# Kernel tuning notes

Hardware: AMD Instinct MI355X
Metric: run time of the kernel (lower is better)

Reference implementation:

```python
import jax, jax.numpy as jnp
from jax import lax
import numpy as np

H = W = 224
N = H * W
T = 25          # landscape sample points
K_MAX = 2       # number of landscapes
M_PTS = 64      # max persistence-diagram points kept (top persistence)
OUT_F = 50
CHUNK = 512     # pixels per DTM chunk


def _make_offsets(m0):
    # static, sorted-by-distance local window covering >= m0 fraction of mass for near-uniform weights
    r = int(np.ceil(np.sqrt(m0 * N / np.pi) * 1.3))
    dy, dx = np.meshgrid(np.arange(-r, r + 1), np.arange(-r, r + 1), indexing="ij")
    d2 = (dy * dy + dx * dx).astype(np.float32).ravel()
    o = np.argsort(d2, kind="stable")
    return jnp.asarray(dy.ravel()[o]), jnp.asarray(dx.ravel()[o]), jnp.asarray(d2[o]), r

_OFF = {m0: _make_offsets(m0) for m0 in (0.05, 0.2)}


def _dtm(w_img, m0):
    """Weighted distance-to-measure on the unit-spacing 224x224 grid.
    dtm(x)^2 = (1/(m0*W)) * sum of w_j * d_j^2 over nearest grid points until cumulative
    weight reaches m0*W (partial weight on the crossing point). Offsets are pre-sorted by
    distance (identical for every pixel), so no per-pixel sort is needed."""
    dy, dx, d2, r = _OFF[m0]
    B = w_img.shape[0]
    wp = jnp.pad(w_img, ((0, 0), (r, r), (r, r)))
    thr = m0 * w_img.sum(axis=(1, 2))                      # (B,)
    pix = jnp.arange(N).reshape(N // CHUNK, CHUNK)

    def body(p):
        y = p // W + r
        x = p % W + r
        vals = wp[:, y[:, None] + dy[None, :], x[:, None] + dx[None, :]]  # (B,C,O)
        c = jnp.cumsum(vals, axis=-1)
        used = jnp.minimum(jnp.maximum(thr[:, None, None] - (c - vals), 0.0), vals)
        return jnp.einsum("bco,o->bc", used, d2) / thr[:, None]

    dtm2 = lax.map(jax.checkpoint(body), pix)              # (n_chunks, B, CHUNK)
    return jnp.sqrt(jnp.maximum(dtm2.transpose(1, 0, 2).reshape(B, N), 0.0))


def _h0_pairs_np(f_batch):
    """0-dim persistent homology (sublevel filtration, 4-connectivity) via union-find.
    Returns indices of birth/death pixels so birth/death VALUES can be gathered
    differentiably in jax (PLLay-style gradients)."""
    f_batch = np.asarray(f_batch)
    B = f_batch.shape[0]
    b_idx = np.zeros((B, M_PTS), np.int32)
    d_idx = np.zeros((B, M_PTS), np.int32)
    mask = np.zeros((B, M_PTS), np.bool_)
    for bb in range(B):
        f = f_batch[bb]
        order = np.argsort(f, kind="stable")
        parent = np.full(N, -1, np.int64)
        pairs = []
        for i in order:
            i = int(i)
            parent[i] = i
            y, x = divmod(i, W)
            nbs = []
            if y > 0: nbs.append(i - W)
            if y < H - 1: nbs.append(i + W)
            if x > 0: nbs.append(i - 1)
            if x < W - 1: nbs.append(i + 1)
            for nb in nbs:
                if parent[nb] < 0:
                    continue
                ri = i
                while parent[ri] != ri:
                    parent[ri] = parent[parent[ri]]; ri = parent[ri]
                rn = nb
                while parent[rn] != rn:
                    parent[rn] = parent[parent[rn]]; rn = parent[rn]
                if ri == rn:
                    continue
                if f[ri] <= f[rn]:
                    elder, young = ri, rn
                else:
                    elder, young = rn, ri
                pairs.append((young, i))   # elder rule: younger component dies here
                parent[young] = elder
        pairs.append((int(np.argmin(f)), int(np.argmax(f))))  # essential class
        pa = np.asarray(pairs, np.int64)
        pers = f[pa[:, 1]] - f[pa[:, 0]]
        keep = np.argsort(-pers)[:M_PTS]
        k = len(keep)
        b_idx[bb, :k] = pa[keep, 0]
        d_idx[bb, :k] = pa[keep, 1]
        mask[bb, :k] = pers[keep] > 0
    return b_idx, d_idx, mask


def _topo_layer(x_img, m0, tseq, gw, gb):
    # AdTopoLayer: DTM -> H0 persistence diagram -> persistence landscapes at tseq -> Linear
    dt = _dtm(x_img, m0)                                   # (B, N)
    B = dt.shape[0]
    shapes = (jax.ShapeDtypeStruct((B, M_PTS), np.int32),
              jax.ShapeDtypeStruct((B, M_PTS), np.int32),
              jax.ShapeDtypeStruct((B, M_PTS), np.bool_))
    b_idx, d_idx, mask = jax.pure_callback(_h0_pairs_np, shapes, lax.stop_gradient(dt))
    birth = jnp.take_along_axis(dt, b_idx, axis=1)         # differentiable gather
    death = jnp.take_along_axis(dt, d_idx, axis=1)
    death = jnp.where(mask, death, birth)                  # invalid slots -> zero tent
    t = tseq[None, None, :]                                # (1,1,T)
    tents = jnp.maximum(jnp.minimum(t - birth[:, :, None], death[:, :, None] - t), 0.0)
    lam, _ = lax.top_k(tents.transpose(0, 2, 1), K_MAX)    # (B,T,K): k-th largest tents
    feat = lam.transpose(0, 2, 1).reshape(B, K_MAX * T)    # (B,50)
    return feat @ gw.T + gb


def _forward(input, params):
    xs = []
    for m0, g in ((0.05, "1"), (0.2, "2")):
        for c in range(3):
            n = "t" + g + str(c + 1)
            xs.append(_topo_layer(input[:, c], m0, params[n + "_tseq"], params[n + "_w"], params[n + "_b"]))
    x = jnp.concatenate(xs, axis=-1)                       # (B, 300)
    signal = jnp.abs(lax.stop_gradient(x)).sum(axis=0)     # (300,) detached signal
    output = jax.nn.relu(x) @ params["fc_w"].T + params["fc_b"]
    return output, signal


def setup_inputs():
    key = jax.random.key(0)
    ks = jax.random.split(key, 8)
    B = 2
    inp = {"input": jax.random.uniform(ks[0], (B, 3, H, W), jnp.float32)}
    centers = {"1": 20.0, "2": 40.0}   # typical DTM value ranges for m0=0.05 / 0.2
    i = 1
    for g in ("1", "2"):
        for c in ("1", "2", "3"):
            n = "t" + g + c
            kk = jax.random.fold_in(ks[1], i)
            inp[n + "_tseq"] = jnp.linspace(centers[g] - 15.0, centers[g] + 15.0, T).astype(jnp.float32)
            inp[n + "_w"] = 0.1 * jax.random.normal(kk, (OUT_F, K_MAX * T), jnp.float32)
            inp[n + "_b"] = jnp.zeros((OUT_F,), jnp.float32)
            i += 1
    inp["fc_w"] = 0.1 * jax.random.normal(ks[2], (7, 6 * OUT_F), jnp.float32)
    inp["fc_b"] = jnp.zeros((7,), jnp.float32)
    return inp


def reference(input, t11_tseq, t11_w, t11_b, t12_tseq, t12_w, t12_b, t13_tseq, t13_w, t13_b, t21_tseq, t21_w, t21_b, t22_tseq, t22_w, t22_b, t23_tseq, t23_w, t23_b, fc_w, fc_b):
    params = dict(t11_tseq=t11_tseq, t11_w=t11_w, t11_b=t11_b,
                  t12_tseq=t12_tseq, t12_w=t12_w, t12_b=t12_b,
                  t13_tseq=t13_tseq, t13_w=t13_w, t13_b=t13_b,
                  t21_tseq=t21_tseq, t21_w=t21_w, t21_b=t21_b,
                  t22_tseq=t22_tseq, t22_w=t22_w, t22_b=t22_b,
                  t23_tseq=t23_tseq, t23_w=t23_w, t23_b=t23_b,
                  fc_w=fc_w, fc_b=fc_b)
    return _forward(input, params)
```

## Files before the change

### kernel.cpp

```cpp
#include <hip/hip_runtime.h>
#include <stdint.h>

#define HWDIM 224
#define NPIX (HWDIM*HWDIM)
#define NFIELD 12
#define TT 25

#define R1v 37
#define PW1v (HWDIM + 2*R1v)
#define R2v 74
#define PW2v (HWDIM + 2*R2v)

#define HSIZE 16384
#define FCAP 4096
#define RHASH 4096
#define DON 36

typedef unsigned long long u64;

struct LayerParams {
    const float* tseq[6];
    const float* gw[6];
    const float* gb[6];
};

constexpr size_t alup(size_t x) { return (x + 255) & ~(size_t)255; }
constexpr size_t SZPA = (size_t)6*PW1v*(PW1v+1)*4;
constexpr size_t SZPB = (size_t)6*PW2v*(PW2v+1)*4;
constexpr size_t OFF_SUMS = 0;
constexpr size_t OFF_P0A = alup(OFF_SUMS + 8*4);
constexpr size_t OFF_PZA = alup(OFF_P0A + SZPA);
constexpr size_t OFF_P0B = alup(OFF_PZA + 2*SZPA);
constexpr size_t OFF_PZB = alup(OFF_P0B + SZPB);
constexpr size_t OFF_DT   = alup(OFF_PZB + 2*SZPB);
constexpr size_t OFF_KEY  = alup(OFF_DT   + (size_t)NFIELD*NPIX*4);
constexpr size_t OFF_HP   = alup(OFF_KEY  + (size_t)NFIELD*NPIX*8);
constexpr size_t OFF_HB   = alup(OFF_HP   + (size_t)NFIELD*HSIZE*8);
constexpr size_t OFF_X    = alup(OFF_HB   + (size_t)NFIELD*HSIZE*8);


__global__ __launch_bounds__(1024) void k_sums(const float* __restrict__ inp, float* __restrict__ sums) {
    int img = blockIdx.x;
    const float* p = inp + (size_t)img * NPIX;
    __shared__ float red[1024];
    float s = 0.f;
    for (int i = threadIdx.x; i < NPIX; i += 1024) s += p[i];
    red[threadIdx.x] = s; __syncthreads();
    for (int w = 512; w > 0; w >>= 1) {
        if (threadIdx.x < w) red[threadIdx.x] += red[threadIdx.x + w];
        __syncthreads();
    }
    if (threadIdx.x == 0) sums[img] = red[0];
}

__global__ __launch_bounds__(64) void k_prefix(const float* __restrict__ inp,
        float* __restrict__ p0a, float2* __restrict__ pza,
        float* __restrict__ p0b, float2* __restrict__ pzb) {
    int bidx = blockIdx.x;
    const int tot0 = 6 * PW1v;
    int g = (bidx >= tot0);
    int rem = g ? (bidx - tot0) : bidx;
    const int PW = g ? PW2v : PW1v, R = g ? R2v : R1v, C = PW + 1;
    int img = rem / PW, row = rem % PW;
    float* P0 = (g ? p0b : p0a) + ((size_t)img*PW + row) * C;
    float2* PZ = (g ? pzb : pza) + ((size_t)img*PW + row) * C;
    int iy = row - R;
    bool rowok = ((unsigned)iy < HWDIM);
    const float* src = inp + (size_t)img*NPIX + (size_t)(rowok ? iy : 0)*HWDIM;
    const int lane = threadIdx.x;
    if (lane == 0) { P0[0] = 0.f; PZ[0] = make_float2(0.f, 0.f); }
    float c0 = 0.f, c1 = 0.f, c2 = 0.f;
    for (int i = 0; i < 6; ++i) {
        int k = i*64 + lane;
        float v = 0.f;
        if (k < PW && rowok) { int ix = k - R; if ((unsigned)ix < HWDIM) v = src[ix]; }
        float xd = (float)k;
        float w0 = v, w1 = v*xd, w2 = v*xd*xd;
        #pragma unroll
        for (int off = 1; off < 64; off <<= 1) {
            float t0 = __shfl_up(w0, off), t1 = __shfl_up(w1, off), t2 = __shfl_up(w2, off);
            if (lane >= off) { w0 += t0; w1 += t1; w2 += t2; }
        }
        if (k < PW) {
            P0[k+1] = c0 + w0;
            PZ[k+1] = make_float2(c1 + w1, c2 + w2);
        }
        c0 += __shfl(w0, 63); c1 += __shfl(w1, 63); c2 += __shfl(w2, 63);
    }
}

__device__ __forceinline__ int k_init_exact(int X, int R) {
    int K = (int)sqrtf((float)X) + 1;
    if (K > R) K = R;
    while (K > 0 && K*K > X) --K;
    return K;
}

__device__ __forceinline__ float dmass1(int X, const float* __restrict__ P0, int bidx,
        int C, int R) {
    float m = 0.f;
    int K = 0;
    if (X >= 0) {
        K = k_init_exact(X, R);
        m = P0[bidx+K+1] - P0[bidx-K];
    }
    int t = X - 1, step = 3;
    const float* __restrict__ Pu = P0 - C;
    const float* __restrict__ Pd = P0 + C;
    for (int dyy = 1; dyy <= R; ++dyy) {
        if (__all(t < 0)) break;
        if (t >= 0) {
            while (K*K > t) --K;
            int A = bidx + K + 1, B = bidx - K;
            m += (Pu[A] - Pu[B]) + (Pd[A] - Pd[B]);
        }
        t -= step; step += 2; Pu -= C; Pd += C;
    }
    return m;
}

__global__ __launch_bounds__(256) void k_dtm(const float* __restrict__ sums,
        const float* __restrict__ p0a, const float2* __restrict__ pza,
        const float* __restrict__ p0b, const float2* __restrict__ pzb,
        float* __restrict__ dt, u64* __restrict__ key) {
    const int xcd = blockIdx.x & 7, slot = blockIdx.x >> 3;
    int f, blk;
    if (xcd < 6) {
        if (slot < 196)            { f = 6 + xcd; blk = slot; }
        else if (slot < 196 + DON) { f = xcd; blk = (196 - DON) + (slot - 196); }
        else return;
    } else {
        const int per = 196 - DON;
        if (slot >= 3*per) return;
        int q = slot / per;
        f = (xcd - 6)*3 + q; blk = slot - q*per;
    }
    const int layer = f >> 1, b = f & 1;
    const int g = layer / 3, c = layer % 3;
    const int img = b*3 + c;
    const int R = g ? R2v : R1v, PW = g ? PW2v : PW1v, C = PW + 1;
    const int R2 = 2*R*R;
    const float thr = (g ? 0.2f : 0.05f) * sums[img];
    const float* __restrict__ P0 = (g ? p0b : p0a) + (size_t)img*PW*C;
    const float2* __restrict__ PZ = (g ? pzb : pza) + (size_t)img*PW*C;

    const int p = blk*256 + threadIdx.x;
    const int y = p / HWDIM, x = p % HWDIM;
    const int xc = x + R;
    const int bidx = (y + R)*C + xc;

    const int NP = g ? 7 : 6;
    const int WSTOP = g ? 86 : 43;
    int lo = 0, hi = R2 + 1;
    for (int it = 0; it < NP; ++it) {
        int X = (lo + hi) >> 1;
        float m = dmass1(X, P0, bidx, C, R);
        if (m >= thr) hi = X; else lo = X + 1;
    }
    for (int rit = 0; rit < 14; ++rit) {
        bool act = (hi == R2 + 1) ? (lo < hi) : (hi - lo > WSTOP);
        if (__all(!act)) break;
        int X = act ? ((lo + hi) >> 1) : -1;
        float m = dmass1(X, P0, bidx, C, R);
        if (X >= 0) { if (m >= thr) hi = X; else lo = X + 1; }
    }
    const bool nr = (hi == R2 + 1);
    const int  Dst = nr ? lo : ((lo + hi) >> 1);
    const bool cross = nr ? (lo <= R2) : true;
    const int  Xin = cross ? (Dst - 1) : R2;

    float m_in = 0.f, ws = 0.f;
    const float c2n = -2.f * (float)xc;
    const int xc2i = xc * xc;
    int K = 0;
    if (Xin >= 0) {
        K = k_init_exact(Xin, R);
        int A = bidx+K+1, B = bidx-K;
        float s0 = P0[A] - P0[B]; float2 zA = PZ[A], zB = PZ[B];
        m_in += s0; ws += fmaf((float)xc2i, s0, fmaf(c2n, zA.x - zB.x, zA.y - zB.y));
    }
    {
        int t = Xin - 1, step = 3, d2 = 1;
        const float* __restrict__ Pu = P0 - C;
        const float* __restrict__ Pd = P0 + C;
        const float2* __restrict__ Zu = PZ - C;
        const float2* __restrict__ Zd = PZ + C;
        for (int dyy = 1; dyy <= R; ++dyy) {
            if (__all(t < 0)) break;
            if (t >= 0) {
                while (K*K > t) --K;
                int A = bidx+K+1, B = bidx-K;
                float c1 = (float)(d2 + xc2i);
                { float s0 = Pu[A]-Pu[B]; float2 zA = Zu[A], zB = Zu[B];
                  m_in += s0; ws += fmaf(c1, s0, fmaf(c2n, zA.x - zB.x, zA.y - zB.y)); }
                { float s0 = Pd[A]-Pd[B]; float2 zA = Zd[A], zB = Zd[B];
                  m_in += s0; ws += fmaf(c1, s0, fmaf(c2n, zA.x - zB.x, zA.y - zB.y)); }
            }
            t -= step; d2 += step; step += 2;
            Pu -= C; Pd += C; Zu -= C; Zd += C;
        }
    }
    float s = cross ? (ws + (float)Dst * (thr - m_in)) : ws;
    float d = sqrtf(fmaxf(s / thr, 0.f));
    dt[(size_t)f*NPIX + p] = d;
    key[(size_t)f*NPIX + p] = ((u64)__float_as_uint(d) << 32) | (unsigned)p;
}

__device__ inline unsigned hash64(u64 x) {
    x ^= x >> 33; x *= 0xff51afd7ed558ccdULL;
    x ^= x >> 33; x *= 0xc4ceb9fe1a85ec53ULL;
    x ^= x >> 33;
    return (unsigned)x;
}

struct FinSh {
    u64 ek[FCAP];
    unsigned int epk[FCAP];
    unsigned int eab[FCAP];
    unsigned short eru[FCAP];
    int rhk[RHASH];
    short ufp[RHASH];
    float rdt[RHASH];
    unsigned int pyd[FCAP];
    float ppr[FCAP];
};

__device__ __forceinline__ void bitonic_n(u64* ek, int tid, int n, int bst) {
    for (int k = 2; k <= n; k <<= 1) {
        for (int j = k >> 1; j > 0; j >>= 1) {
            for (int i = tid; i < n; i += bst) {
                int ixj = i ^ j;
                if (ixj > i) {
                    u64 a = ek[i], b = ek[ixj];
                    if (((i & k) == 0) ? (a > b) : (a < b)) { ek[i] = b; ek[ixj] = a; }
                }
            }
            __syncthreads();
        }
    }
}

__global__ __launch_bounds__(1024) void k_fused(const float* __restrict__ dt,
        const u64* __restrict__ key,
        u64* __restrict__ hpair, u64* __restrict__ hbest,
        LayerParams lp, float* __restrict__ xbuf) {
    const int xcd = blockIdx.x & 7, slot = blockIdx.x >> 3;
    int f;
    if (xcd < 6) { if (slot != 0) return; f = 6 + xcd; }
    else f = (xcd - 6)*3 + slot;
    const int layer = f >> 1, bb = f & 1;
    const int tid = threadIdx.x; const int bs = 1024;
    const float* dtf = dt + (size_t)f*NPIX;
    const u64* kf = key + (size_t)f*NPIX;
    u64* hp = hpair + (size_t)f*HSIZE;
    u64* hb = hbest + (size_t)f*HSIZE;

    __shared__ union U {
        unsigned short par[NPIX];
        FinSh fin;
    } sh;
    __shared__ float birth[64], death[64], featsh[2*TT];
    __shared__ int spec_a[64], spec_b[64];
    __shared__ u64 spec_e[64];
    __shared__ int cnt_s, pc_s;
    __shared__ int gmin_s, gmax_s; __shared__ float gminf_s, gmaxf_s;

    u64 mymin = ~0ull, mymax = 0;
    for (int p = tid; p < NPIX; p += bs) {
        u64 kp = kf[p]; u64 best = kp; int bi = p;
        const int y = p / HWDIM, x = p % HWDIM;
        if (y > 0)        { u64 t = kf[p - HWDIM]; if (t < best) { best = t; bi = p - HWDIM; } }
        if (y < HWDIM-1)  { u64 t = kf[p + HWDIM]; if (t < best) { best = t; bi = p + HWDIM; } }
        if (x > 0)        { u64 t = kf[p - 1];     if (t < best) { best = t; bi = p - 1; } }
        if (x < HWDIM-1)  { u64 t = kf[p + 1];     if (t < best) { best = t; bi = p + 1; } }
        sh.par[p] = (unsigned short)bi;
        if (kp < mymin) mymin = kp;
        u64 mk = (kp & 0xFFFFFFFF00000000ull) | (0xFFFFu - (unsigned)(kp & 0xFFFFu));
        if (mk > mymax) mymax = mk;
    }
    {
        u64* red = (u64*)sh.fin.pyd;
        red[tid] = mymin; red[1024 + tid] = mymax;
        __syncthreads();
        for (int w = 512; w > 0; w >>= 1) {
            if (tid < w) {
                if (red[tid + w] < red[tid]) red[tid] = red[tid + w];
                if (red[1024 + tid + w] > red[1024 + tid]) red[1024 + tid] = red[1024 + tid + w];
            }
            __syncthreads();
        }
        if (tid == 0) {
            gmin_s = (int)(unsigned)(red[0] & 0xFFFFu);
            gminf_s = __uint_as_float((unsigned)(red[0] >> 32));
            gmax_s = 0xFFFF - (int)(unsigned)(red[1024] & 0xFFFFu);
            gmaxf_s = __uint_as_float((unsigned)(red[1024] >> 32));
            cnt_s = 0; pc_s = 0;
        }
    }
    __syncthreads();
    for (int pass = 0; pass < 6; ++pass) {
        for (int p = tid; p < NPIX; p += bs) sh.par[p] = sh.par[sh.par[p]];
        __syncthreads();
    }
    for (int p = tid; p < NPIX; p += bs) {
        int a = sh.par[p];
        int n = sh.par[a];
        while (n != a) { a = n; n = sh.par[a]; }
        sh.par[p] = (unsigned short)a;
    }
    __syncthreads();
    for (int p = tid; p < NPIX; p += bs) {
        const int rp = sh.par[p];
        const int y = p / HWDIM, x = p % HWDIM;
        const u64 kp = kf[p];
        #pragma unroll
        for (int e = 0; e < 2; ++e) {
            int q;
            if (e == 0) { if (x >= HWDIM-1) continue; q = p + 1; }
            else        { if (y >= HWDIM-1) continue; q = p + HWDIM; }
            int rq = sh.par[q];
            if (rq == rp) continue;
            u64 kq = kf[q];
            u64 kmax; int ru;
            if (kp > kq) { kmax = kp; ru = rp; } else { kmax = kq; ru = rq; }
            u64 ekv = (kmax & 0xFFFFFFFF00000000ull) | ((kmax & 0xFFFFull) << 16) | (unsigned)ru;
            int ra = min(rp, rq), rb = max(rp, rq);
            u64 pk = ((u64)(unsigned)ra << 32) | (unsigned)rb;
            unsigned h = hash64(pk) & (HSIZE - 1);
            for (int probe = 0; probe < HSIZE; ++probe) {
                u64 old = atomicCAS(&hp[h], ~0ull, pk);
                if (old == ~0ull || old == pk) { atomicMin(&hb[h], ekv); break; }
                h = (h + 1) & (HSIZE - 1);
            }
        }
    }
    __syncthreads();
    for (int i = tid; i < RHASH; i += bs) sh.fin.rhk[i] = -1;
    __syncthreads();
    for (int i = tid; i < HSIZE; i += bs) {
        u64 pk = hp[i];
        if (pk != ~0ull) {
            int slot2 = atomicAdd(&cnt_s, 1);
            if (slot2 < FCAP) {
                u64 e = hb[i];
                unsigned u = (unsigned)((e >> 16) & 0xFFFFu);
                unsigned ru = (unsigned)(e & 0xFFFFu);
                sh.fin.ek[slot2] = (e & 0xFFFFFFFF00000000ull) | ((u64)u << 16) | (unsigned)slot2;
                int ra = (int)(pk >> 32), rb = (int)(pk & 0xFFFFFFFFu);
                sh.fin.epk[slot2] = ((unsigned)ra << 16) | (unsigned)rb;
                sh.fin.eru[slot2] = (unsigned short)ru;
                #pragma unroll
                for (int pass = 0; pass < 2; ++pass) {
                    int r = pass ? rb : ra;
                    unsigned h = ((unsigned)r * 2654435761u) & (RHASH - 1);
                    for (int pr = 0; pr < RHASH; ++pr) {
                        int old = atomicCAS(&sh.fin.rhk[h], -1, r);
                        if (old == -1 || old == r) break;
                        h = (h + 1) & (RHASH - 1);
                    }
                }
            }
        }
    }
    __syncthreads();
    int cnt = min(cnt_s, FCAP);
    int n1 = 64; while (n1 < cnt) n1 <<= 1;
    for (int s2 = tid; s2 < cnt; s2 += bs) {
        unsigned pk2 = sh.fin.epk[s2];
        int ra = (int)(pk2 >> 16), rb = (int)(pk2 & 0xFFFFu);
        int ru = sh.fin.eru[s2];
        int rv = (ru == ra) ? rb : ra;
        int su = -1, sv = -1;
        { unsigned h = ((unsigned)ru * 2654435761u) & (RHASH - 1);
          for (int pr = 0; pr < RHASH; ++pr) { int v = sh.fin.rhk[h]; if (v == ru) { su = (int)h; break; } if (v == -1) break; h = (h + 1) & (RHASH - 1); } }
        { unsigned h = ((unsigned)rv * 2654435761u) & (RHASH - 1);
          for (int pr = 0; pr < RHASH; ++pr) { int v = sh.fin.rhk[h]; if (v == rv) { sv = (int)h; break; } if (v == -1) break; h = (h + 1) & (RHASH - 1); } }
        sh.fin.eab[s2] = ((unsigned)su << 16) | (unsigned)(sv & 0xFFFF);
    }
    for (int i = cnt + tid; i < n1; i += bs) sh.fin.ek[i] = ~0ull;
    for (int s2 = tid; s2 < RHASH; s2 += bs) {
        sh.fin.ufp[s2] = (short)s2;
        int r = sh.fin.rhk[s2];
        sh.fin.rdt[s2] = (r >= 0) ? dtf[r] : 0.f;
    }
    __syncthreads();

    bitonic_n(sh.fin.ek, tid, n1, bs);

    if (tid < 64) {
        int pc = 0;
        for (int base = 0; base < cnt; base += 64) {
            int i = base + tid;
            int sa = -1, sb = -1; u64 e = ~0ull;
            if (i < cnt) {
                e = sh.fin.ek[i];
                int idx = (int)(e & 0xFFFFu);
                unsigned ab = sh.fin.eab[idx];
                sa = (int)(ab >> 16); sb = (int)(ab & 0xFFFFu);
                if (sa != 0xFFFF && sb != 0xFFFF) {
                    while (sh.fin.ufp[sa] != sa) { short g2 = sh.fin.ufp[sh.fin.ufp[sa]]; sh.fin.ufp[sa] = g2; sa = g2; }
                    while (sh.fin.ufp[sb] != sb) { short g2 = sh.fin.ufp[sh.fin.ufp[sb]]; sh.fin.ufp[sb] = g2; sb = g2; }
                    if (sa == sb) sa = -1;
                } else { sa = -1; }
            }
            spec_a[tid] = sa; spec_b[tid] = sb; spec_e[tid] = e;
            if (tid == 0) {
                int lim = min(64, cnt - base);
                for (int j = 0; j < lim; ++j) {
                    int sa2 = spec_a[j];
                    if (sa2 < 0) continue;
                    int sb2 = spec_b[j];
                    u64 e2 = spec_e[j];
                    while (sh.fin.ufp[sa2] != sa2) { short g2 = sh.fin.ufp[sh.fin.ufp[sa2]]; sh.fin.ufp[sa2] = g2; sa2 = g2; }
                    while (sh.fin.ufp[sb2] != sb2) { short g2 = sh.fin.ufp[sh.fin.ufp[sb2]]; sh.fin.ufp[sb2] = g2; sb2 = g2; }
                    if (sa2 == sb2) continue;
                    float fa = sh.fin.rdt[sa2], fb = sh.fin.rdt[sb2];
                    int elder, young;
                    if (fa <= fb) { elder = sa2; young = sb2; } else { elder = sb2; young = sa2; }
                    sh.fin.ufp[young] = (short)elder;
                    float pers = __uint_as_float((unsigned)(e2 >> 32)) - sh.fin.rdt[young];
                    if (pers > 0.f && pc < FCAP - 1) {
                        int u = (int)((e2 >> 16) & 0xFFFFu);
                        sh.fin.pyd[pc] = ((unsigned)sh.fin.rhk[young] << 16) | (unsigned)u;
                        sh.fin.ppr[pc] = pers; ++pc;
                    }
                }
            }
        }
        if (tid == 0) {
            sh.fin.pyd[pc] = ((unsigned)gmin_s << 16) | (unsigned)gmax_s;
            sh.fin.ppr[pc] = gmaxf_s - gminf_s; ++pc;
            pc_s = pc;
        }
    }
    __syncthreads();
    const int pc = pc_s;
    int n2 = 64; while (n2 < pc) n2 <<= 1;

    for (int i = tid; i < n2; i += bs) {
        if (i < pc && sh.fin.ppr[i] > 0.f)
            sh.fin.ek[i] = ((u64)(0xFFFFFFFFu - __float_as_uint(sh.fin.ppr[i])) << 32) | (unsigned)i;
        else sh.fin.ek[i] = ~0ull;
    }
    __syncthreads();
    bitonic_n(sh.fin.ek, tid, n2, bs);
    if (tid < 64) {
        u64 e = sh.fin.ek[tid];
        int bpix = 0, dpix = 0, msk = 0;
        if (e != ~0ull) {
            int i = (int)(e & 0xFFFFFFFFu);
            unsigned pd2 = sh.fin.pyd[i];
            bpix = (int)(pd2 >> 16); dpix = (int)(pd2 & 0xFFFFu); msk = 1;
        }
        float bv = dtf[bpix];
        float dv = msk ? dtf[dpix] : bv;
        birth[tid] = bv; death[tid] = dv;
    }
    __syncthreads();
    if (tid < TT) {
        float t = lp.tseq[layer][tid];
        float m1 = 0.f, m2 = 0.f;
        for (int m = 0; m < 64; ++m) {
            float v = fmaxf(fminf(t - birth[m], death[m] - t), 0.f);
            if (v > m1) { m2 = m1; m1 = v; } else if (v > m2) m2 = v;
        }
        featsh[tid] = m1; featsh[TT + tid] = m2;
    }
    __syncthreads();
    if (tid < 50) {
        const float* w = lp.gw[layer] + tid * 50;
        float acc = lp.gb[layer][tid];
        #pragma unroll
        for (int j = 0; j < 50; ++j) acc = fmaf(featsh[j], w[j], acc);
        xbuf[bb*300 + layer*50 + tid] = acc;
    }
}

__global__ __launch_bounds__(512) void k_final(const float* __restrict__ x, const float* __restrict__ fcw,
        const float* __restrict__ fcb, float* __restrict__ out) {
    __shared__ float rl[2][300];
    const int tid = threadIdx.x;
    if (tid < 300) {
        float a0 = x[tid], a1 = x[300 + tid];
        out[14 + tid] = fabsf(a0) + fabsf(a1);
        rl[0][tid] = fmaxf(a0, 0.f);
        rl[1][tid] = fmaxf(a1, 0.f);
    }
    __syncthreads();
    if (tid < 14) {
        int b = tid / 7, i = tid % 7;
        float acc = fcb[i];
        const float* w = fcw + i * 300;
        for (int j = 0; j < 300; ++j) acc = fmaf(rl[b][j], w[j], acc);
        out[b*7 + i] = acc;
    }
}

extern "C" void kernel_launch(void* const* d_in, const int* in_sizes, int n_in,
                              void* d_out, int out_size, void* d_ws, size_t ws_size,
                              hipStream_t stream) {
    (void)in_sizes; (void)n_in; (void)out_size; (void)ws_size;
    const float* inp = (const float*)d_in[0];
    LayerParams lp;
    for (int l = 0; l < 6; ++l) {
        lp.tseq[l] = (const float*)d_in[1 + 3*l];
        lp.gw[l]   = (const float*)d_in[2 + 3*l];
        lp.gb[l]   = (const float*)d_in[3 + 3*l];
    }
    const float* fcw = (const float*)d_in[19];
    const float* fcb = (const float*)d_in[20];

    char* w = (char*)d_ws;
    float* sums = (float*)(w + OFF_SUMS);
    float* p0a = (float*)(w + OFF_P0A);
    float2* pza = (float2*)(w + OFF_PZA);
    float* p0b = (float*)(w + OFF_P0B);
    float2* pzb = (float2*)(w + OFF_PZB);
    float* dt = (float*)(w + OFF_DT);
    u64* key = (u64*)(w + OFF_KEY);
    u64* hp = (u64*)(w + OFF_HP);
    u64* hb = (u64*)(w + OFF_HB);
    float* xbuf = (float*)(w + OFF_X);

    hipLaunchKernelGGL(k_sums, dim3(6), dim3(1024), 0, stream, inp, sums);
    const int prefRows = 6*PW1v + 6*PW2v;
    hipLaunchKernelGGL(k_prefix, dim3(prefRows), dim3(64), 0, stream,
                       inp, p0a, pza, p0b, pzb);
    hipMemsetAsync(hp, 0xFF, (size_t)2*NFIELD*HSIZE*8, stream);
    const int maxslot = 3 * (196 - DON);
    hipLaunchKernelGGL(k_dtm, dim3(8 * maxslot), dim3(256), 0, stream,
                       sums, p0a, pza, p0b, pzb, dt, key);
    hipLaunchKernelGGL(k_fused, dim3(24), dim3(1024), 0, stream,
                       dt, key, hp, hb, lp, xbuf);
    hipLaunchKernelGGL(k_final, dim3(1), dim3(512), 0, stream, xbuf, fcw, fcb, (float*)d_out);
}
```

Measured before the change: 758.5 us.

## Move steepest-descent parent and min/max reduction out of fused kernel into wide grid

The per-pixel lowest-neighbour parent computation and the global min/max key reduction move out of the 12-block fused kernel into a new fully parallel kernel (196x12 blocks), which writes 16-bit parents and atomically reduced extremes to global memory. The 64-bit key array is dropped; keys are rebuilt from the float distance field when needed. Image sums now come from the last column of the row prefix sums instead of a separate pass over the input. The cost is an extra launch and global traffic for the parent array, in exchange for far more parallelism than the few large blocks had.

```diff
diff --git a/kernel.cpp b/kernel.cpp
--- a/kernel.cpp
+++ b/kernel.cpp
@@ -33,25 +33,12 @@
 constexpr size_t OFF_P0B = alup(OFF_PZA + 2*SZPA);
 constexpr size_t OFF_PZB = alup(OFF_P0B + SZPB);
 constexpr size_t OFF_DT   = alup(OFF_PZB + 2*SZPB);
-constexpr size_t OFF_KEY  = alup(OFF_DT   + (size_t)NFIELD*NPIX*4);
-constexpr size_t OFF_HP   = alup(OFF_KEY  + (size_t)NFIELD*NPIX*8);
+constexpr size_t OFF_PAR  = alup(OFF_DT   + (size_t)NFIELD*NPIX*4);
+constexpr size_t OFF_HP   = alup(OFF_PAR  + (size_t)NFIELD*NPIX*2);
 constexpr size_t OFF_HB   = alup(OFF_HP   + (size_t)NFIELD*HSIZE*8);
-constexpr size_t OFF_X    = alup(OFF_HB   + (size_t)NFIELD*HSIZE*8);
-
-
-__global__ __launch_bounds__(1024) void k_sums(const float* __restrict__ inp, float* __restrict__ sums) {
-    int img = blockIdx.x;
-    const float* p = inp + (size_t)img * NPIX;
-    __shared__ float red[1024];
-    float s = 0.f;
-    for (int i = threadIdx.x; i < NPIX; i += 1024) s += p[i];
-    red[threadIdx.x] = s; __syncthreads();
-    for (int w = 512; w > 0; w >>= 1) {
-        if (threadIdx.x < w) red[threadIdx.x] += red[threadIdx.x + w];
-        __syncthreads();
-    }
-    if (threadIdx.x == 0) sums[img] = red[0];
-}
+constexpr size_t OFF_GMM  = OFF_HB + (size_t)NFIELD*HSIZE*8;
+constexpr size_t OFF_X    = alup(OFF_GMM + 256);
+
 
 __global__ __launch_bounds__(64) void k_prefix(const float* __restrict__ inp,
         float* __restrict__ p0a, float2* __restrict__ pza,
@@ -89,6 +76,22 @@
     }
 }
 
+__global__ __launch_bounds__(256) void k_sums2(const float* __restrict__ p0a,
+        float* __restrict__ sums) {
+    int img = blockIdx.x;
+    __shared__ float red[256];
+    float s = 0.f;
+    const int C = PW1v + 1;
+    for (int r = threadIdx.x; r < PW1v; r += 256)
+        s += p0a[((size_t)img*PW1v + r)*C + PW1v];
+    red[threadIdx.x] = s; __syncthreads();
+    for (int w = 128; w > 0; w >>= 1) {
+        if (threadIdx.x < w) red[threadIdx.x] += red[threadIdx.x + w];
+        __syncthreads();
+    }
+    if (threadIdx.x == 0) sums[img] = red[0];
+}
+
 __device__ __forceinline__ int k_init_exact(int X, int R) {
     int K = (int)sqrtf((float)X) + 1;
     if (K > R) K = R;
@@ -122,7 +125,7 @@
 __global__ __launch_bounds__(256) void k_dtm(const float* __restrict__ sums,
         const float* __restrict__ p0a, const float2* __restrict__ pza,
         const float* __restrict__ p0b, const float2* __restrict__ pzb,
-        float* __restrict__ dt, u64* __restrict__ key) {
+        float* __restrict__ dt) {
     const int xcd = blockIdx.x & 7, slot = blockIdx.x >> 3;
     int f, blk;
     if (xcd < 6) {
@@ -203,7 +206,37 @@
     float s = cross ? (ws + (float)Dst * (thr - m_in)) : ws;
     float d = sqrtf(fmaxf(s / thr, 0.f));
     dt[(size_t)f*NPIX + p] = d;
-    key[(size_t)f*NPIX + p] = ((u64)__float_as_uint(d) << 32) | (unsigned)p;
+}
+
+__global__ __launch_bounds__(256) void k_desc(const float* __restrict__ dt,
+        unsigned short* __restrict__ par, u64* __restrict__ gmm) {
+    const int f = blockIdx.y;
+    const int p = blockIdx.x*256 + threadIdx.x;
+    const float* __restrict__ dtf = dt + (size_t)f*NPIX;
+    float dc = dtf[p];
+    u64 kc = ((u64)__float_as_uint(dc) << 32) | (unsigned)p;
+    u64 best = kc; int bi = p;
+    const int y = p / HWDIM, x = p % HWDIM;
+    if (y > 0)        { float v = dtf[p - HWDIM]; u64 t = ((u64)__float_as_uint(v)<<32)|(unsigned)(p-HWDIM); if (t < best) { best = t; bi = p-HWDIM; } }
+    if (y < HWDIM-1)  { float v = dtf[p + HWDIM]; u64 t = ((u64)__float_as_uint(v)<<32)|(unsigned)(p+HWDIM); if (t < best) { best = t; bi = p+HWDIM; } }
+    if (x > 0)        { float v = dtf[p - 1];     u64 t = ((u64)__float_as_uint(v)<<32)|(unsigned)(p-1);     if (t < best) { best = t; bi = p-1; } }
+    if (x < HWDIM-1)  { float v = dtf[p + 1];     u64 t = ((u64)__float_as_uint(v)<<32)|(unsigned)(p+1);     if (t < best) { best = t; bi = p+1; } }
+    par[(size_t)f*NPIX + p] = (unsigned short)bi;
+    __shared__ u64 rmin[256], rmax[256];
+    u64 mk = ((u64)__float_as_uint(dc) << 32) | (unsigned)(0xFFFF - p);
+    rmin[threadIdx.x] = kc; rmax[threadIdx.x] = mk;
+    __syncthreads();
+    for (int w = 128; w > 0; w >>= 1) {
+        if (threadIdx.x < w) {
+            if (rmin[threadIdx.x + w] < rmin[threadIdx.x]) rmin[threadIdx.x] = rmin[threadIdx.x + w];
+            if (rmax[threadIdx.x + w] > rmax[threadIdx.x]) rmax[threadIdx.x] = rmax[threadIdx.x + w];
+        }
+        __syncthreads();
+    }
+    if (threadIdx.x == 0) {
+        atomicMin(&gmm[f*2 + 0], rmin[0]);
+        atomicMin(&gmm[f*2 + 1], ~rmax[0]);
+    }
 }
 
 __device__ inline unsigned hash64(u64 x) {
@@ -241,7 +274,7 @@
 }
 
 __global__ __launch_bounds__(1024) void k_fused(const float* __restrict__ dt,
-        const u64* __restrict__ key,
+        const unsigned short* __restrict__ parg, const u64* __restrict__ gmm,
         u64* __restrict__ hpair, u64* __restrict__ hbest,
         LayerParams lp, float* __restrict__ xbuf) {
     const int xcd = blockIdx.x & 7, slot = blockIdx.x >> 3;
@@ -251,7 +284,6 @@
     const int layer = f >> 1, bb = f & 1;
     const int tid = threadIdx.x; const int bs = 1024;
     const float* dtf = dt + (size_t)f*NPIX;
-    const u64* kf = key + (size_t)f*NPIX;
     u64* hp = hpair + (size_t)f*HSIZE;
     u64* hb = hbest + (size_t)f*HSIZE;
 
@@ -265,37 +297,19 @@
     __shared__ int cnt_s, pc_s;
     __shared__ int gmin_s, gmax_s; __shared__ float gminf_s, gmaxf_s;
 
-    u64 mymin = ~0ull, mymax = 0;
-    for (int p = tid; p < NPIX; p += bs) {
-        u64 kp = kf[p]; u64 best = kp; int bi = p;
-        const int y = p / HWDIM, x = p % HWDIM;
-        if (y > 0)        { u64 t = kf[p - HWDIM]; if (t < best) { best = t; bi = p - HWDIM; } }
-        if (y < HWDIM-1)  { u64 t = kf[p + HWDIM]; if (t < best) { best = t; bi = p + HWDIM; } }
-        if (x > 0)        { u64 t = kf[p - 1];     if (t < best) { best = t; bi = p - 1; } }
-        if (x < HWDIM-1)  { u64 t = kf[p + 1];     if (t < best) { best = t; bi = p + 1; } }
-        sh.par[p] = (unsigned short)bi;
-        if (kp < mymin) mymin = kp;
-        u64 mk = (kp & 0xFFFFFFFF00000000ull) | (0xFFFFu - (unsigned)(kp & 0xFFFFu));
-        if (mk > mymax) mymax = mk;
-    }
     {
-        u64* red = (u64*)sh.fin.pyd;
-        red[tid] = mymin; red[1024 + tid] = mymax;
-        __syncthreads();
-        for (int w = 512; w > 0; w >>= 1) {
-            if (tid < w) {
-                if (red[tid + w] < red[tid]) red[tid] = red[tid + w];
-                if (red[1024 + tid + w] > red[1024 + tid]) red[1024 + tid] = red[1024 + tid + w];
-            }
-            __syncthreads();
-        }
-        if (tid == 0) {
-            gmin_s = (int)(unsigned)(red[0] & 0xFFFFu);
-            gminf_s = __uint_as_float((unsigned)(red[0] >> 32));
-            gmax_s = 0xFFFF - (int)(unsigned)(red[1024] & 0xFFFFu);
-            gmaxf_s = __uint_as_float((unsigned)(red[1024] >> 32));
-            cnt_s = 0; pc_s = 0;
-        }
+        const unsigned* src = (const unsigned*)(parg + (size_t)f*NPIX);
+        unsigned* dst = (unsigned*)sh.par;
+        for (int i = tid; i < NPIX/2; i += bs) dst[i] = src[i];
+    }
+    if (tid == 0) {
+        u64 g0v = gmm[f*2 + 0];
+        u64 g1v = ~gmm[f*2 + 1];
+        gmin_s = (int)(unsigned)(g0v & 0xFFFFFFFFu);
+        gminf_s = __uint_as_float((unsigned)(g0v >> 32));
+        gmax_s = 0xFFFF - (int)(g1v & 0xFFFFu);
+        gmaxf_s = __uint_as_float((unsigned)(g1v >> 32));
+        cnt_s = 0; pc_s = 0;
     }
     __syncthreads();
     for (int pass = 0; pass < 6; ++pass) {
@@ -312,7 +326,7 @@
     for (int p = tid; p < NPIX; p += bs) {
         const int rp = sh.par[p];
         const int y = p / HWDIM, x = p % HWDIM;
-        const u64 kp = kf[p];
+        const float dp = dtf[p];
         #pragma unroll
         for (int e = 0; e < 2; ++e) {
             int q;
@@ -320,10 +334,11 @@
             else        { if (y >= HWDIM-1) continue; q = p + HWDIM; }
             int rq = sh.par[q];
             if (rq == rp) continue;
-            u64 kq = kf[q];
-            u64 kmax; int ru;
-            if (kp > kq) { kmax = kp; ru = rp; } else { kmax = kq; ru = rq; }
-            u64 ekv = (kmax & 0xFFFFFFFF00000000ull) | ((kmax & 0xFFFFull) << 16) | (unsigned)ru;
+            float dq = dtf[q];
+            bool pdies = (dp > dq) || (dp == dq && p > q);
+            u64 ekv = pdies
+                ? (((u64)__float_as_uint(dp) << 32) | ((u64)(unsigned)p << 16) | (unsigned)rp)
+                : (((u64)__float_as_uint(dq) << 32) | ((u64)(unsigned)q << 16) | (unsigned)rq);
             int ra = min(rp, rq), rb = max(rp, rq);
             u64 pk = ((u64)(unsigned)ra << 32) | (unsigned)rb;
             unsigned h = hash64(pk) & (HSIZE - 1);
@@ -517,20 +532,22 @@
     float* p0b = (float*)(w + OFF_P0B);
     float2* pzb = (float2*)(w + OFF_PZB);
     float* dt = (float*)(w + OFF_DT);
-    u64* key = (u64*)(w + OFF_KEY);
+    unsigned short* par = (unsigned short*)(w + OFF_PAR);
     u64* hp = (u64*)(w + OFF_HP);
     u64* hb = (u64*)(w + OFF_HB);
+    u64* gmm = (u64*)(w + OFF_GMM);
     float* xbuf = (float*)(w + OFF_X);
 
-    hipLaunchKernelGGL(k_sums, dim3(6), dim3(1024), 0, stream, inp, sums);
     const int prefRows = 6*PW1v + 6*PW2v;
     hipLaunchKernelGGL(k_prefix, dim3(prefRows), dim3(64), 0, stream,
                        inp, p0a, pza, p0b, pzb);
-    hipMemsetAsync(hp, 0xFF, (size_t)2*NFIELD*HSIZE*8, stream);
+    hipLaunchKernelGGL(k_sums2, dim3(6), dim3(256), 0, stream, p0a, sums);
+    hipMemsetAsync(hp, 0xFF, (size_t)2*NFIELD*HSIZE*8 + 256, stream);
     const int maxslot = 3 * (196 - DON);
     hipLaunchKernelGGL(k_dtm, dim3(8 * maxslot), dim3(256), 0, stream,
-                       sums, p0a, pza, p0b, pzb, dt, key);
+                       sums, p0a, pza, p0b, pzb, dt);
+    hipLaunchKernelGGL(k_desc, dim3(NPIX/256, NFIELD), dim3(256), 0, stream, dt, par, gmm);
     hipLaunchKernelGGL(k_fused, dim3(24), dim3(1024), 0, stream,
-                       dt, key, hp, hb, lp, xbuf);
+                       dt, par, gmm, hp, hb, lp, xbuf);
     hipLaunchKernelGGL(k_final, dim3(1), dim3(512), 0, stream, xbuf, fcw, fcb, (float*)d_out);
 }
```

Result: faster. 721.7 us (-4.8%).
